# Kernel tuning notes

Measured on AMD Instinct MI355X. Metric: run time of the kernel, lower is better.

Reference implementation:

```python
import jax, jax.numpy as jnp
import numpy as np

N_HEADS = 12

def setup_inputs() -> dict:
    key = jax.random.key(0)
    k1, k2, k3 = jax.random.split(key, 3)
    B, N, D = 2, 2048, 768
    x = jax.random.normal(k1, (B, N, D), dtype=jnp.float32)
    # Linear weights stored as [in, out] (equivalent to torch W.T)
    Wkqv = jax.random.normal(k2, (D, 3 * D), dtype=jnp.float32) * (1.0 / np.sqrt(D))
    bkqv = jnp.zeros((3 * D,), dtype=jnp.float32)
    Wproj = jax.random.normal(k3, (D, D), dtype=jnp.float32) * (1.0 / np.sqrt(D))
    bproj = jnp.zeros((D,), dtype=jnp.float32)
    return {"x": x, "Wkqv": Wkqv, "bkqv": bkqv, "Wproj": Wproj, "bproj": bproj}


def reference(x, Wkqv, bkqv, Wproj, bproj):
    B, N, D = x.shape
    H = N_HEADS
    hd = D // H
    kqv = x @ Wkqv + bkqv                     # [B, N, 3D]
    # NOTE: original chunks in (k, q, v) order
    k, q, v = jnp.split(kqv, 3, axis=-1)
    k = k.reshape(B, N, H, hd).transpose(0, 2, 1, 3)   # [B, H, N, hd]
    q = q.reshape(B, N, H, hd).transpose(0, 2, 1, 3)
    v = v.reshape(B, N, H, hd).transpose(0, 2, 1, 3)
    att = jnp.einsum('bhqd,bhkd->bhqk', q, k) / jnp.sqrt(jnp.float32(hd))
    causal = jnp.tril(jnp.ones((N, N), dtype=bool))    # [N, N]
    att = jnp.where(causal[None, None, :, :], att, jnp.float32(-jnp.inf))
    w = jax.nn.softmax(att, axis=-1)
    sa = jnp.einsum('bhqk,bhkd->bhqd', w, v)           # [B, H, N, hd]
    sa = sa.transpose(0, 2, 1, 3).reshape(B, N, D)
    return sa @ Wproj + bproj
```

## Files before the change

### kernel.cpp

```cpp
#include <hip/hip_runtime.h>

typedef __attribute__((ext_vector_type(8))) short bf16x8;
typedef __attribute__((ext_vector_type(4))) float f32x4;
typedef __attribute__((ext_vector_type(16))) float f32x16;

#define BATCH 2
#define SEQ 2048
#define DMODEL 768
#define NH 12
#define HD 64
#define M_TOK (BATCH * SEQ)
#define N_KQV (3 * DMODEL)

#define GLOAD16(gsrc, ldst) __builtin_amdgcn_global_load_lds( \
    (const __attribute__((address_space(1))) unsigned int*)(const void*)(gsrc), \
    (__attribute__((address_space(3))) unsigned int*)(void*)(ldst), 16, 0, 0)

__device__ __forceinline__ unsigned short f2bf(float f) {
  unsigned int u = __float_as_uint(f);
  u += 0x7FFFu + ((u >> 16) & 1u);
  return (unsigned short)(u >> 16);
}

__device__ __forceinline__ unsigned int cvtpk(float lo, float hi) {
  unsigned int r;
  asm("v_cvt_pk_bf16_f32 %0, %1, %2" : "=v"(r) : "v"(lo), "v"(hi));
  return r;
}

#define NB_CVT 3072
#define NB_T1 (72 * 24)
#define NB_T2 (24 * 24)

__global__ __launch_bounds__(256) void prep_kernel(
    const float* __restrict__ x, unsigned short* __restrict__ x_bf,
    const float* __restrict__ Wkqv, unsigned short* __restrict__ wkqvT,
    const float* __restrict__ Wproj, unsigned short* __restrict__ wprojT) {
  const int b = blockIdx.x;
  if (b < NB_CVT) {
    int i = b * 256 + threadIdx.x;
    float4 v = reinterpret_cast<const float4*>(x)[i];
    unsigned long long p = (unsigned long long)f2bf(v.x)
                         | ((unsigned long long)f2bf(v.y) << 16)
                         | ((unsigned long long)f2bf(v.z) << 32)
                         | ((unsigned long long)f2bf(v.w) << 48);
    reinterpret_cast<unsigned long long*>(x_bf)[i] = p;
    return;
  }
  __shared__ float tile[32][33];
  const float* in;
  unsigned short* out;
  int rows, cols, bx, by;
  if (b < NB_CVT + NB_T1) {
    int j = b - NB_CVT;
    in = Wkqv; out = wkqvT; rows = DMODEL; cols = N_KQV;
    bx = j % 72; by = j / 72;
  } else {
    int j = b - NB_CVT - NB_T1;
    in = Wproj; out = wprojT; rows = DMODEL; cols = DMODEL;
    bx = j % 24; by = j / 24;
  }
  const int tx = threadIdx.x & 31, ty = threadIdx.x >> 5;
  int c0 = bx * 32, r0 = by * 32;
  for (int i = ty; i < 32; i += 8)
    tile[i][tx] = in[(size_t)(r0 + i) * cols + c0 + tx];
  __syncthreads();
  for (int i = ty; i < 32; i += 8)
    out[(size_t)(c0 + i) * rows + r0 + tx] = f2bf(tile[tx][i]);
}

template <int BM, int BN, int MODE>
__global__ __launch_bounds__(256) void gemm_bt(
    const unsigned short* __restrict__ A,
    const unsigned short* __restrict__ BT,
    const float* __restrict__ bias,
    int M, int N, int K,
    unsigned short* __restrict__ outK, unsigned short* __restrict__ outQ,
    unsigned short* __restrict__ outVT, float* __restrict__ outF) {
  constexpr int MI = BM / 64;
  constexpr int NJ = BN / 64;
  constexpr int L = BM / 64 + BN / 64;
  __shared__ __align__(16) unsigned short lds_a[3][BM][32];
  __shared__ __align__(16) unsigned short lds_b[3][BN][32];
  const int tid = threadIdx.x;
  const int lane = tid & 63;
  const int w = tid >> 6;
  const int wm = w >> 1, wn = w & 1;
  const int l31 = lane & 31, hi = lane >> 5;
  const int m0 = blockIdx.y * BM, n0 = blockIdx.x * BN;

  f32x16 acc[MI][NJ];
#pragma unroll
  for (int mi = 0; mi < MI; mi++)
#pragma unroll
    for (int nj = 0; nj < NJ; nj++)
#pragma unroll
      for (int i = 0; i < 16; i++) acc[mi][nj][i] = 0.f;

  const int srow = lane >> 2;
  const int sg = ((lane & 3) ^ ((lane >> 3) & 3)) * 8;
  const int xq = (l31 >> 1) & 3;

#define STAGE(buf, k0)                                                        \
  {                                                                           \
    _Pragma("unroll")                                                         \
    for (int rr = 0; rr < BM / 64; ++rr)                                      \
      GLOAD16(&A[(size_t)(m0 + rr * 64 + w * 16 + srow) * K + (k0) + sg],     \
              &lds_a[buf][rr * 64 + w * 16][0]);                              \
    _Pragma("unroll")                                                         \
    for (int rr = 0; rr < BN / 64; ++rr)                                      \
      GLOAD16(&BT[(size_t)(n0 + rr * 64 + w * 16 + srow) * K + (k0) + sg],    \
              &lds_b[buf][rr * 64 + w * 16][0]);                              \
  }

  const int KT = K >> 5;
  STAGE(0, 0);
  STAGE(1, 32);

  int cur = 0;
  for (int kt = 0; kt < KT; ++kt) {
    if (kt + 1 < KT) {
      if constexpr (L == 4)      asm volatile("s_waitcnt vmcnt(4)" ::: "memory");
      else if constexpr (L == 3) asm volatile("s_waitcnt vmcnt(3)" ::: "memory");
      else                       asm volatile("s_waitcnt vmcnt(2)" ::: "memory");
    } else {
      asm volatile("s_waitcnt vmcnt(0)" ::: "memory");
    }
    __builtin_amdgcn_s_barrier();
    __builtin_amdgcn_sched_barrier(0);

    bf16x8 aA[2][MI], aB[2][NJ];
#pragma unroll
    for (int ds = 0; ds < 2; ds++) {
      const int rc = ((ds * 2 + hi) ^ xq) * 8;
#pragma unroll
      for (int mi = 0; mi < MI; mi++)
        aA[ds][mi] = *(const bf16x8*)&lds_a[cur][wm * (BM / 2) + mi * 32 + l31][rc];
#pragma unroll
      for (int nj = 0; nj < NJ; nj++)
        aB[ds][nj] = *(const bf16x8*)&lds_b[cur][wn * (BN / 2) + nj * 32 + l31][rc];
    }
#pragma unroll
    for (int ds = 0; ds < 2; ds++)
#pragma unroll
      for (int mi = 0; mi < MI; mi++)
#pragma unroll
        for (int nj = 0; nj < NJ; nj++)
          acc[mi][nj] = __builtin_amdgcn_mfma_f32_32x32x16_bf16(
              aA[ds][mi], aB[ds][nj], acc[mi][nj], 0, 0, 0);

    if (kt + 2 < KT) {
      const int nb = (cur + 2 >= 3) ? cur - 1 : cur + 2;
      STAGE(nb, (kt + 2) << 5);
    }
    cur = (cur == 2) ? 0 : cur + 1;
  }
#undef STAGE

#pragma unroll
  for (int mi = 0; mi < MI; mi++) {
#pragma unroll
    for (int nj = 0; nj < NJ; nj++) {
#pragma unroll
      for (int r = 0; r < 16; r++) {
        int row = m0 + wm * (BM / 2) + mi * 32 + (r & 3) + 8 * (r >> 2) + 4 * hi;
        int col = n0 + wn * (BN / 2) + nj * 32 + l31;
        float v = acc[mi][nj][r] + bias[col];
        if (MODE == 0) {
          int chunk = col / DMODEL;
          int d = col - chunk * DMODEL;
          int hh = d >> 6, di = d & 63;
          int bb = row >> 11, tok = row & 2047;
          int bh = bb * NH + hh;
          if (chunk == 0)
            outK[((size_t)bh * SEQ + tok) * HD + di] = f2bf(v);
          else if (chunk == 1)
            outQ[((size_t)bh * SEQ + tok) * HD + di] = f2bf(v * 0.125f);
          else
            outVT[((size_t)bh * HD + di) * SEQ + tok] = f2bf(v);
        } else {
          outF[(size_t)row * N + col] = v;
        }
      }
    }
  }
}

__global__ __launch_bounds__(128) void attn_kernel(
    const unsigned short* __restrict__ qbuf,
    const unsigned short* __restrict__ kbuf,
    const unsigned short* __restrict__ vT,
    unsigned short* __restrict__ sa) {
  __shared__ __align__(16) char smem_raw[18432];
  auto k_lds = reinterpret_cast<unsigned short (*)[72]>(smem_raw);
  auto v_lds = reinterpret_cast<unsigned short (*)[72]>(smem_raw + 9216);
  auto o_merge = reinterpret_cast<float (*)[32][33]>(smem_raw);
  auto l_merge = reinterpret_cast<float (*)[32]>(smem_raw + 9216);

  const int tid = threadIdx.x, lane = tid & 63, w = tid >> 6;
  const int l31 = lane & 31, hi = lane >> 5;

  const int fid = (int)blockIdx.y * (int)gridDim.x + (int)blockIdx.x;
  const int xcd = fid & 7, slot = fid >> 3;
  const int head3 = slot % 3;
  const int t = 63 - slot / 3;
  const int bh = head3 * 8 + xcd;
  const int ktmax = t >> 1;

  const size_t qk_base = (size_t)bh * SEQ * HD;
  const size_t v_base = (size_t)bh * HD * SEQ;
  const int bb = bh / NH, h = bh - bb * NH;

  const int sr = w * 32 + (lane >> 3);
  const int sc = (lane & 7) * 8;

  {
    bf16x8 rk[4], rv[4];
#pragma unroll
    for (int p = 0; p < 4; p++) {
      rk[p] = *(const bf16x8*)&kbuf[qk_base + (size_t)(sr + 8 * p) * HD + sc];
      rv[p] = *(const bf16x8*)&vT[v_base + (size_t)(sr + 8 * p) * SEQ + sc];
    }
#pragma unroll
    for (int p = 0; p < 4; p++) {
      *(bf16x8*)&k_lds[sr + 8 * p][sc] = rk[p];
      *(bf16x8*)&v_lds[sr + 8 * p][sc] = rv[p];
    }
  }

  bf16x8 aq[4];
#pragma unroll
  for (int ds = 0; ds < 4; ds++)
    aq[ds] = *(const bf16x8*)&qbuf[qk_base + (size_t)(t * 32 + l31) * HD + ds * 16 + hi * 8];

  f32x16 o0, o1;
#pragma unroll
  for (int i = 0; i < 16; i++) { o0[i] = 0.f; o1[i] = 0.f; }
  float lsum = 0.f;

  __syncthreads();

  for (int kt = 0; kt <= ktmax; ++kt) {
    const bool more = (kt < ktmax);
    bf16x8 rk[4], rv[4];
    if (more) {
      const int nrow = (kt + 1) * 64;
#pragma unroll
      for (int p = 0; p < 4; p++) {
        rk[p] = *(const bf16x8*)&kbuf[qk_base + (size_t)(nrow + sr + 8 * p) * HD + sc];
        rv[p] = *(const bf16x8*)&vT[v_base + (size_t)(sr + 8 * p) * SEQ + nrow + sc];
      }
    }

    f32x16 s;
#pragma unroll
    for (int i = 0; i < 16; i++) s[i] = 0.f;
    __builtin_amdgcn_s_setprio(1);
#pragma unroll
    for (int ds = 0; ds < 4; ds++) {
      bf16x8 bk = *(const bf16x8*)&k_lds[w * 32 + l31][ds * 16 + hi * 8];
      s = __builtin_amdgcn_mfma_f32_32x32x16_bf16(bk, aq[ds], s, 0, 0, 0);
    }
    __builtin_amdgcn_s_setprio(0);

    const bool diag = (kt == ktmax);
    const int qb2 = (t & 1) * 32;
#pragma unroll
    for (int r = 0; r < 16; r++) {
      int kr = (r & 3) + 8 * (r >> 2) + 4 * hi;
      float val = s[r];
      if (diag && (w * 32 + kr > qb2 + l31)) val = -1e30f;
      float p = __expf(val);
      s[r] = p;
      lsum += p;
    }

    union { unsigned int u[4]; bf16x8 v; } f1, f2;
    {
      unsigned int A = cvtpk(s[0], s[1]), B = cvtpk(s[2], s[3]);
      unsigned int C = cvtpk(s[4], s[5]), D = cvtpk(s[6], s[7]);
      auto rAC = __builtin_amdgcn_permlane32_swap(A, C, false, false);
      auto rBD = __builtin_amdgcn_permlane32_swap(B, D, false, false);
      f1.u[0] = rAC[0]; f1.u[1] = rBD[0]; f1.u[2] = rAC[1]; f1.u[3] = rBD[1];
      unsigned int A2 = cvtpk(s[8], s[9]),   B2 = cvtpk(s[10], s[11]);
      unsigned int C2 = cvtpk(s[12], s[13]), D2 = cvtpk(s[14], s[15]);
      auto rAC2 = __builtin_amdgcn_permlane32_swap(A2, C2, false, false);
      auto rBD2 = __builtin_amdgcn_permlane32_swap(B2, D2, false, false);
      f2.u[0] = rAC2[0]; f2.u[1] = rBD2[0]; f2.u[2] = rAC2[1]; f2.u[3] = rBD2[1];
    }

    __builtin_amdgcn_s_setprio(1);
    {
      bf16x8 bv00 = *(const bf16x8*)&v_lds[l31][w * 32 + hi * 8];
      bf16x8 bv01 = *(const bf16x8*)&v_lds[32 + l31][w * 32 + hi * 8];
      o0 = __builtin_amdgcn_mfma_f32_32x32x16_bf16(f1.v, bv00, o0, 0, 0, 0);
      o1 = __builtin_amdgcn_mfma_f32_32x32x16_bf16(f1.v, bv01, o1, 0, 0, 0);
      bf16x8 bv10 = *(const bf16x8*)&v_lds[l31][w * 32 + 16 + hi * 8];
      bf16x8 bv11 = *(const bf16x8*)&v_lds[32 + l31][w * 32 + 16 + hi * 8];
      o0 = __builtin_amdgcn_mfma_f32_32x32x16_bf16(f2.v, bv10, o0, 0, 0, 0);
      o1 = __builtin_amdgcn_mfma_f32_32x32x16_bf16(f2.v, bv11, o1, 0, 0, 0);
    }
    __builtin_amdgcn_s_setprio(0);

    if (more) {
      __syncthreads();
#pragma unroll
      for (int p = 0; p < 4; p++) {
        *(bf16x8*)&k_lds[sr + 8 * p][sc] = rk[p];
        *(bf16x8*)&v_lds[sr + 8 * p][sc] = rv[p];
      }
      __syncthreads();
    }
  }

  __syncthreads();
  {
    float ltot = lsum + __shfl_xor(lsum, 32);
    if (hi == 0) l_merge[w][l31] = ltot;
    f32x16 osend = w ? o0 : o1;
#pragma unroll
    for (int r = 0; r < 16; r++) {
      int ql = (r & 3) + 8 * (r >> 2) + 4 * hi;
      o_merge[w][ql][l31] = osend[r];
    }
    __syncthreads();
    f32x16 okeep = w ? o1 : o0;
#pragma unroll
    for (int r = 0; r < 16; r++) {
      int ql = (r & 3) + 8 * (r >> 2) + 4 * hi;
      float ot = okeep[r] + o_merge[1 - w][ql][l31];
      float lt = l_merge[0][ql] + l_merge[1][ql];
      sa[((size_t)bb * SEQ + t * 32 + ql) * DMODEL + h * HD + w * 32 + l31] = f2bf(ot / lt);
    }
  }
}


extern "C" void kernel_launch(void* const* d_in, const int* in_sizes, int n_in,
                              void* d_out, int out_size, void* d_ws, size_t ws_size,
                              hipStream_t stream) {
  const float* x     = (const float*)d_in[0];
  const float* Wkqv  = (const float*)d_in[1];
  const float* bkqv  = (const float*)d_in[2];
  const float* Wproj = (const float*)d_in[3];
  const float* bproj = (const float*)d_in[4];
  float* out = (float*)d_out;

  char* ws = (char*)d_ws;
  unsigned short* x_bf   = (unsigned short*)(ws + 0);
  unsigned short* wkqvT  = (unsigned short*)(ws + 6291456);
  unsigned short* wprojT = (unsigned short*)(ws + 9830400);
  unsigned short* qb     = (unsigned short*)(ws + 11010048);
  unsigned short* kb     = (unsigned short*)(ws + 17301504);
  unsigned short* vT     = (unsigned short*)(ws + 23592960);
  unsigned short* sa     = (unsigned short*)(ws + 29884416);

  prep_kernel<<<NB_CVT + NB_T1 + NB_T2, 256, 0, stream>>>(
      x, x_bf, Wkqv, wkqvT, Wproj, wprojT);

  gemm_bt<128, 128, 0><<<dim3(N_KQV / 128, M_TOK / 128), 256, 0, stream>>>(
      x_bf, wkqvT, bkqv, M_TOK, N_KQV, DMODEL, kb, qb, vT, nullptr);

  attn_kernel<<<dim3(64, BATCH * NH), 128, 0, stream>>>(qb, kb, vT, sa);

  gemm_bt<64, 64, 1><<<dim3(DMODEL / 64, M_TOK / 64), 256, 0, stream>>>(
      sa, wprojT, bproj, M_TOK, DMODEL, DMODEL, nullptr, nullptr, nullptr, out);
}
```

Baseline: 103.0 us.

## Use 8-wave 128x128 GEMM blocks for both QKV and output projections

Replaces the templated 4-wave GEMM with an 8-wave, 512-thread kernel on a fixed 128x128 tile. Each wave now computes a 32x64 sub-tile, and waves are split between loading A and loading B. The output projection moves from 64x64 tiles to 128x128 tiles, which gives fewer blocks (192) with more waves each. The aim is more waves per CU to hide latency and less redundant operand loading, at the cost of less MFMA work per wave and fewer blocks for the small projection GEMM.

```diff
diff --git a/kernel.cpp b/kernel.cpp
--- a/kernel.cpp
+++ b/kernel.cpp
@@ -69,48 +69,48 @@
     out[(size_t)(c0 + i) * rows + r0 + tx] = f2bf(tile[tx][i]);
 }
 
-template <int BM, int BN, int MODE>
-__global__ __launch_bounds__(256) void gemm_bt(
+template <int MODE>
+__global__ __launch_bounds__(512) void gemm_8w(
     const unsigned short* __restrict__ A,
     const unsigned short* __restrict__ BT,
     const float* __restrict__ bias,
-    int M, int N, int K,
+    int NTOT,
     unsigned short* __restrict__ outK, unsigned short* __restrict__ outQ,
     unsigned short* __restrict__ outVT, float* __restrict__ outF) {
-  constexpr int MI = BM / 64;
-  constexpr int NJ = BN / 64;
-  constexpr int L = BM / 64 + BN / 64;
-  __shared__ __align__(16) unsigned short lds_a[3][BM][32];
-  __shared__ __align__(16) unsigned short lds_b[3][BN][32];
+  constexpr int K = DMODEL;
+  __shared__ __align__(16) unsigned short lds_a[3][128][32];
+  __shared__ __align__(16) unsigned short lds_b[3][128][32];
   const int tid = threadIdx.x;
   const int lane = tid & 63;
   const int w = tid >> 6;
-  const int wm = w >> 1, wn = w & 1;
+  const int wr = (w & 3) * 32;
+  const int wc = (w >> 2) * 64;
   const int l31 = lane & 31, hi = lane >> 5;
-  const int m0 = blockIdx.y * BM, n0 = blockIdx.x * BN;
-
-  f32x16 acc[MI][NJ];
-#pragma unroll
-  for (int mi = 0; mi < MI; mi++)
-#pragma unroll
-    for (int nj = 0; nj < NJ; nj++)
-#pragma unroll
-      for (int i = 0; i < 16; i++) acc[mi][nj][i] = 0.f;
+  const int m0 = blockIdx.y * 128, n0 = blockIdx.x * 128;
+
+  f32x16 acc[2];
+#pragma unroll
+  for (int nj = 0; nj < 2; nj++)
+#pragma unroll
+    for (int i = 0; i < 16; i++) acc[nj][i] = 0.f;
 
   const int srow = lane >> 2;
   const int sg = ((lane & 3) ^ ((lane >> 3) & 3)) * 8;
   const int xq = (l31 >> 1) & 3;
 
-#define STAGE(buf, k0)                                                        \
-  {                                                                           \
-    _Pragma("unroll")                                                         \
-    for (int rr = 0; rr < BM / 64; ++rr)                                      \
-      GLOAD16(&A[(size_t)(m0 + rr * 64 + w * 16 + srow) * K + (k0) + sg],     \
-              &lds_a[buf][rr * 64 + w * 16][0]);                              \
-    _Pragma("unroll")                                                         \
-    for (int rr = 0; rr < BN / 64; ++rr)                                      \
-      GLOAD16(&BT[(size_t)(n0 + rr * 64 + w * 16 + srow) * K + (k0) + sg],    \
-              &lds_b[buf][rr * 64 + w * 16][0]);                              \
+#define STAGE(buf, k0)                                                         \
+  {                                                                            \
+    if (w < 4) {                                                               \
+      GLOAD16(&A[(size_t)(m0 + w * 32 + srow) * K + (k0) + sg],                \
+              &lds_a[buf][w * 32][0]);                                         \
+      GLOAD16(&A[(size_t)(m0 + w * 32 + 16 + srow) * K + (k0) + sg],           \
+              &lds_a[buf][w * 32 + 16][0]);                                    \
+    } else {                                                                   \
+      GLOAD16(&BT[(size_t)(n0 + (w - 4) * 32 + srow) * K + (k0) + sg],         \
+              &lds_b[buf][(w - 4) * 32][0]);                                   \
+      GLOAD16(&BT[(size_t)(n0 + (w - 4) * 32 + 16 + srow) * K + (k0) + sg],    \
+              &lds_b[buf][(w - 4) * 32 + 16][0]);                              \
+    }                                                                          \
   }
 
   const int KT = K >> 5;
@@ -119,35 +119,25 @@
 
   int cur = 0;
   for (int kt = 0; kt < KT; ++kt) {
-    if (kt + 1 < KT) {
-      if constexpr (L == 4)      asm volatile("s_waitcnt vmcnt(4)" ::: "memory");
-      else if constexpr (L == 3) asm volatile("s_waitcnt vmcnt(3)" ::: "memory");
-      else                       asm volatile("s_waitcnt vmcnt(2)" ::: "memory");
-    } else {
-      asm volatile("s_waitcnt vmcnt(0)" ::: "memory");
-    }
+    if (kt + 1 < KT) asm volatile("s_waitcnt vmcnt(2)" ::: "memory");
+    else             asm volatile("s_waitcnt vmcnt(0)" ::: "memory");
     __builtin_amdgcn_s_barrier();
     __builtin_amdgcn_sched_barrier(0);
 
-    bf16x8 aA[2][MI], aB[2][NJ];
+    bf16x8 aA[2], aB[2][2];
 #pragma unroll
     for (int ds = 0; ds < 2; ds++) {
       const int rc = ((ds * 2 + hi) ^ xq) * 8;
-#pragma unroll
-      for (int mi = 0; mi < MI; mi++)
-        aA[ds][mi] = *(const bf16x8*)&lds_a[cur][wm * (BM / 2) + mi * 32 + l31][rc];
-#pragma unroll
-      for (int nj = 0; nj < NJ; nj++)
-        aB[ds][nj] = *(const bf16x8*)&lds_b[cur][wn * (BN / 2) + nj * 32 + l31][rc];
+      aA[ds] = *(const bf16x8*)&lds_a[cur][wr + l31][rc];
+#pragma unroll
+      for (int nj = 0; nj < 2; nj++)
+        aB[ds][nj] = *(const bf16x8*)&lds_b[cur][wc + nj * 32 + l31][rc];
     }
 #pragma unroll
     for (int ds = 0; ds < 2; ds++)
 #pragma unroll
-      for (int mi = 0; mi < MI; mi++)
-#pragma unroll
-        for (int nj = 0; nj < NJ; nj++)
-          acc[mi][nj] = __builtin_amdgcn_mfma_f32_32x32x16_bf16(
-              aA[ds][mi], aB[ds][nj], acc[mi][nj], 0, 0, 0);
+      for (int nj = 0; nj < 2; nj++)
+        acc[nj] = __builtin_amdgcn_mfma_f32_32x32x16_bf16(aA[ds], aB[ds][nj], acc[nj], 0, 0, 0);
 
     if (kt + 2 < KT) {
       const int nb = (cur + 2 >= 3) ? cur - 1 : cur + 2;
@@ -158,29 +148,26 @@
 #undef STAGE
 
 #pragma unroll
-  for (int mi = 0; mi < MI; mi++) {
-#pragma unroll
-    for (int nj = 0; nj < NJ; nj++) {
-#pragma unroll
-      for (int r = 0; r < 16; r++) {
-        int row = m0 + wm * (BM / 2) + mi * 32 + (r & 3) + 8 * (r >> 2) + 4 * hi;
-        int col = n0 + wn * (BN / 2) + nj * 32 + l31;
-        float v = acc[mi][nj][r] + bias[col];
-        if (MODE == 0) {
-          int chunk = col / DMODEL;
-          int d = col - chunk * DMODEL;
-          int hh = d >> 6, di = d & 63;
-          int bb = row >> 11, tok = row & 2047;
-          int bh = bb * NH + hh;
-          if (chunk == 0)
-            outK[((size_t)bh * SEQ + tok) * HD + di] = f2bf(v);
-          else if (chunk == 1)
-            outQ[((size_t)bh * SEQ + tok) * HD + di] = f2bf(v * 0.125f);
-          else
-            outVT[((size_t)bh * HD + di) * SEQ + tok] = f2bf(v);
-        } else {
-          outF[(size_t)row * N + col] = v;
-        }
+  for (int nj = 0; nj < 2; nj++) {
+#pragma unroll
+    for (int r = 0; r < 16; r++) {
+      int row = m0 + wr + (r & 3) + 8 * (r >> 2) + 4 * hi;
+      int col = n0 + wc + nj * 32 + l31;
+      float v = acc[nj][r] + bias[col];
+      if (MODE == 0) {
+        int chunk = col / DMODEL;
+        int d = col - chunk * DMODEL;
+        int hh = d >> 6, di = d & 63;
+        int bb = row >> 11, tok = row & 2047;
+        int bh = bb * NH + hh;
+        if (chunk == 0)
+          outK[((size_t)bh * SEQ + tok) * HD + di] = f2bf(v);
+        else if (chunk == 1)
+          outQ[((size_t)bh * SEQ + tok) * HD + di] = f2bf(v * 0.125f);
+        else
+          outVT[((size_t)bh * HD + di) * SEQ + tok] = f2bf(v);
+      } else {
+        outF[(size_t)row * NTOT + col] = v;
       }
     }
   }
@@ -358,11 +345,11 @@
   prep_kernel<<<NB_CVT + NB_T1 + NB_T2, 256, 0, stream>>>(
       x, x_bf, Wkqv, wkqvT, Wproj, wprojT);
 
-  gemm_bt<128, 128, 0><<<dim3(N_KQV / 128, M_TOK / 128), 256, 0, stream>>>(
-      x_bf, wkqvT, bkqv, M_TOK, N_KQV, DMODEL, kb, qb, vT, nullptr);
+  gemm_8w<0><<<dim3(N_KQV / 128, M_TOK / 128), 512, 0, stream>>>(
+      x_bf, wkqvT, bkqv, N_KQV, kb, qb, vT, nullptr);
 
   attn_kernel<<<dim3(64, BATCH * NH), 128, 0, stream>>>(qb, kb, vT, sa);
 
-  gemm_bt<64, 64, 1><<<dim3(DMODEL / 64, M_TOK / 64), 256, 0, stream>>>(
-      sa, wprojT, bproj, M_TOK, DMODEL, DMODEL, nullptr, nullptr, nullptr, out);
-}
+  gemm_8w<1><<<dim3(DMODEL / 128, M_TOK / 128), 512, 0, stream>>>(
+      sa, wprojT, bproj, DMODEL, nullptr, nullptr, nullptr, out);
+}
```

After: 100.8 us. 2.1% less time.
